# Optimization experiments

Measured on AMD Instinct MI355X. Metric: run time of the kernel, lower is better.

Reference implementation:

```python
import jax, jax.numpy as jnp
import numpy as np

NB_HEADS = 16
HEAD_DIM = 64
ATTN_LIM = 1024   # L: span of attention over past tokens
BLOCK = 512       # M: query block size
RAMP = 32         # attn_span_len: soft-mask ramp length
BATCH = 8         # sequences; merged leading dim is BATCH*NB_HEADS


def _skew(X, pad_value):
    # X: B x M x L  ->  B x M x (M+L), row i shifted right by i
    B, M, L = X.shape
    X = jnp.pad(X, ((0, 0), (0, 0), (0, M + 1)), constant_values=pad_value)
    X = X.reshape(B, M * (L + M + 1))[:, :-M]
    return X.reshape(B, M, M + L)


def _unskew(X):
    # X: B x M x (M+L)  ->  B x M x L, undo the diagonal shift
    B, M, ML = X.shape
    L = ML - M
    X = X.reshape(B, M * ML)
    X = jnp.pad(X, ((0, 0), (0, M)))
    X = X.reshape(B, M, ML + 1)
    return X[:, :, :L]


def setup_inputs() -> dict:
    key = jax.random.key(0)
    ks = jax.random.split(key, 5)
    B = BATCH * NB_HEADS
    M, L, H = BLOCK, ATTN_LIM, HEAD_DIM
    return {
        "query": jax.random.normal(ks[0], (B, M, H), jnp.float32),
        "key": jax.random.normal(ks[1], (B, M + L, H), jnp.float32),
        "value": jax.random.normal(ks[2], (B, M + L, H), jnp.float32),
        "key_pe": jax.random.normal(ks[3], (1, H, L), jnp.float32),
        "span_val": jax.random.uniform(ks[4], (NB_HEADS, 1, 1), jnp.float32),
    }


def reference(query, key, value, key_pe, span_val):
    B, M, H = query.shape
    L = key_pe.shape[-1]
    # content attention over the (M+L) cache window, unskewed to relative coords
    attn_cont = _unskew(jnp.matmul(query, jnp.swapaxes(key, -1, -2)))  # B x M x L
    attn_pos = jnp.matmul(query, key_pe)                               # B x M x L
    attn = (attn_cont + attn_pos) / jnp.sqrt(jnp.float32(H))
    attn = jax.nn.softmax(attn, axis=-1)
    # adaptive-span soft mask per head (AdaptiveMask), then renormalize
    z = jnp.clip(span_val, 0.0, 1.0)
    template = jnp.arange(1 - L, 1, dtype=jnp.float32)    # linspace(1-L, 0, L)
    mask = jnp.clip((template + z * jnp.float32(L)) / jnp.float32(RAMP) + 1.0,
                    0.0, 1.0)
    attn = attn.reshape(B // NB_HEADS, NB_HEADS, M, L) * mask[None]
    attn = attn / (attn.sum(-1, keepdims=True) + 1e-8)
    attn = attn.reshape(B, M, L)
    # skew back to absolute coords and contract with values
    out = jnp.matmul(_skew(attn, 0.0), value)             # B x M x H
    return out
```

## Files before the change

### kernel.cpp

```cpp
#include <hip/hip_runtime.h>
#include <hip/hip_bf16.h>

typedef __attribute__((ext_vector_type(8))) short short8;
typedef __attribute__((ext_vector_type(4))) float f32x4;

#define MFMA16(a, b, c) __builtin_amdgcn_mfma_f32_16x16x32_bf16((a), (b), (c), 0, 0, 0)
#define QSCALE 0.18033688f
#define EXP2F(x) __builtin_amdgcn_exp2f(x)

__device__ __forceinline__ unsigned short f2bf(float f) {
    unsigned u = __builtin_bit_cast(unsigned, f);
    u += 0x7FFFu + ((u >> 16) & 1u);
    return (unsigned short)(u >> 16);
}
__device__ __forceinline__ unsigned short bfc(float f) {
    return (unsigned short)((__builtin_bit_cast(unsigned, f) + 0x8000u) >> 16);
}

__device__ __forceinline__ short8 pack8(float4 a, float4 b) {
    short8 r;
    r[0] = (short)f2bf(a.x); r[1] = (short)f2bf(a.y);
    r[2] = (short)f2bf(a.z); r[3] = (short)f2bf(a.w);
    r[4] = (short)f2bf(b.x); r[5] = (short)f2bf(b.y);
    r[6] = (short)f2bf(b.z); r[7] = (short)f2bf(b.w);
    return r;
}
__device__ __forceinline__ short8 pack8s(float4 a, float4 b, float s) {
    short8 r;
    r[0] = (short)f2bf(a.x * s); r[1] = (short)f2bf(a.y * s);
    r[2] = (short)f2bf(a.z * s); r[3] = (short)f2bf(a.w * s);
    r[4] = (short)f2bf(b.x * s); r[5] = (short)f2bf(b.y * s);
    r[6] = (short)f2bf(b.z * s); r[7] = (short)f2bf(b.w * s);
    return r;
}

__device__ __forceinline__ void stage16(const void* g, void* l) {
    __builtin_amdgcn_global_load_lds((const __attribute__((address_space(1))) void*)g,
                                     (__attribute__((address_space(3))) void*)l, 16, 0, 0);
}
__device__ __forceinline__ float bpermf(int sa, float v) {
    return __builtin_bit_cast(float,
        __builtin_amdgcn_ds_bpermute(sa, __builtin_bit_cast(int, v)));
}

__global__ void conv_all_kernel(const float* __restrict__ K, const float* __restrict__ V,
                                const float* __restrict__ PE,
                                unsigned short* __restrict__ Kws,
                                unsigned short* __restrict__ Vws,
                                unsigned short* __restrict__ PET) {
    __shared__ unsigned short T[64][72];
    const int blk = blockIdx.x, tid = threadIdx.x;
    if (blk < 6144) {
        int idx = blk * 256 + tid;
        int jl = idx >> 3;
        int e0 = (idx & 7) << 3;
        int x  = (jl & 7) << 3;
        const float* src = K + ((size_t)jl << 6) + (e0 ^ x);
        float4 a = ((const float4*)src)[0], b = ((const float4*)src)[1];
        *(short8*)(Kws + ((size_t)jl << 6) + e0) = pack8(a, b);
    } else if (blk < 9216) {
        int blkv = blk - 6144;
        int b = blkv / 24, vb = blkv - b * 24;
        {
            int j = tid >> 2, h0 = (tid & 3) << 4;
            const float* src = V + ((size_t)(b * 1536 + vb * 64 + j) << 6) + h0;
            float4 a0 = ((const float4*)src)[0], a1 = ((const float4*)src)[1];
            float4 a2 = ((const float4*)src)[2], a3 = ((const float4*)src)[3];
            *(short8*)&T[j][h0]     = pack8(a0, a1);
            *(short8*)&T[j][h0 + 8] = pack8(a2, a3);
        }
        __syncthreads();
        {
            int h = tid & 63, k0 = (tid >> 6) << 4;
            int x = (h & 7) << 3;
            unsigned short* dst = Vws + ((size_t)(b * 24 + vb) << 12) + (h << 6) + k0;
            short8 o0, o1;
#pragma unroll
            for (int u = 0; u < 8; ++u) o0[u] = (short)T[(k0 + u) ^ x][h];
#pragma unroll
            for (int u = 0; u < 8; ++u) o1[u] = (short)T[(k0 + 8 + u) ^ x][h];
            ((short8*)dst)[0] = o0;
            ((short8*)dst)[1] = o1;
        }
    } else {
        int idx = (blk - 9216) * 256 + tid;
        int l = idx >> 6, h = idx & 63;
        PET[idx] = f2bf(PE[(h << 10) | l]);
    }
}

__global__ void pe_only_kernel(const float* __restrict__ pe,
                               unsigned short* __restrict__ pet) {
    int idx = blockIdx.x * 256 + threadIdx.x;
    int l = idx >> 6, h = idx & 63;
    pet[idx] = f2bf(pe[(h << 10) | l]);
}

__global__ __launch_bounds__(256, 4) void attn_v5(
    const float* __restrict__ Qg, const unsigned short* __restrict__ Kws,
    const unsigned short* __restrict__ Vws, const unsigned short* __restrict__ PET,
    const float* __restrict__ SPAN, float* __restrict__ OUT)
{
    __shared__ unsigned short Klds[2][4096];
    __shared__ unsigned short Vlds[2][4096];
    __shared__ unsigned short Wlds[4][1024];

    const int bid = blockIdx.x;
    const int b   = (bid & 7) * 16 + (bid >> 6);
    const int i0  = ((bid >> 3) & 7) << 6;
    const int tid = threadIdx.x, w = tid >> 6, lane = tid & 63;
    const int c16 = lane & 15, g = lane >> 4;

    float z = SPAN[b & 15];
    z = fminf(fmaxf(z, 0.f), 1.f);
    const float mc = z * 32.f + 1.f - 1023.f * 0.03125f;

    short8 qf0, qf1;
    {
        const float* qp = Qg + ((size_t)((b << 9) + i0 + (w << 4) + c16) << 6) + (g << 3);
        qf0 = pack8s(*(const float4*)qp,        *(const float4*)(qp + 4),  QSCALE);
        qf1 = pack8s(*(const float4*)(qp + 32), *(const float4*)(qp + 36), QSCALE);
    }

    const f32x4 zero = {0.f, 0.f, 0.f, 0.f};
    f32x4 Oacc[4] = {zero, zero, zero, zero};
    f32x4 sumw = zero, sume = zero;
    f32x4 Sp[5];

    const char* kbase = (const char*)Kws + (((size_t)b * 1536 + i0) << 7);
    const char* vbase = (const char*)Vws + (((size_t)b * 24 + (i0 >> 6)) << 13);
    const int ubase = w << 10;
    const int loff  = ubase + lane * 16;

    int bsrc[4];
#pragma unroll
    for (int r = 0; r < 4; ++r)
        bsrc[r] = ((lane & 48) | ((c16 - (g << 2) - r) & 15)) << 2;

#define STAGE(bufi, t) do {                                                    \
        const char* kg_ = kbase + (t) * 8192 + loff;                           \
        const char* vg_ = vbase + (t) * 8192 + loff;                           \
        unsigned short* kl_ = &Klds[bufi][ubase >> 1];                         \
        unsigned short* vl_ = &Vlds[bufi][ubase >> 1];                         \
        stage16(kg_, kl_); stage16(kg_ + 4096, kl_ + 2048);                    \
        stage16(vg_, vl_); stage16(vg_ + 4096, vl_ + 2048);                    \
    } while (0)

#define STRIP(dst, lbase) do {                                                 \
        int lr_ = (lbase) + c16;                                               \
        lr_ = lr_ < 0 ? 0 : (lr_ > 1023 ? 1023 : lr_);                         \
        const unsigned short* pp_ = PET + ((lr_ << 6) + (g << 3));             \
        short8 p0_ = *(const short8*)pp_;                                      \
        short8 p1_ = *(const short8*)(pp_ + 32);                               \
        f32x4 a_ = MFMA16(qf0, p0_, zero);                                     \
        dst = MFMA16(qf1, p1_, a_);                                            \
    } while (0)

    STAGE(0, 0);
    { const int lb0 = -(w << 4) - 16; STRIP(Sp[4], lb0); }

    for (int t = 0; t < 17; ++t) {
        const int buf = t & 1;
        __syncthreads();
        if (t < 16) STAGE(buf ^ 1, t + 1);

        const int d0w = (t << 6) - (w << 4);
        const int lb  = d0w - 16;
        const bool edge = (t == 0) || (t == 16);

        __builtin_amdgcn_s_setprio(1);
        f32x4 Sc[4];
        const int xk = (c16 & 7) << 3;
#pragma unroll
        for (int jc = 0; jc < 4; ++jc) {
            const unsigned short* p = &Klds[buf][(jc * 16 + c16) << 6];
            short8 k0 = *(const short8*)(p + ((g << 3) ^ xk));
            short8 k1 = *(const short8*)(p + (((g << 3) + 32) ^ xk));
            f32x4 a = MFMA16(qf0, k0, zero);
            Sc[jc] = MFMA16(qf1, k1, a);
        }
        Sp[0] = Sp[4];
        STRIP(Sp[1], lb + 16);
        STRIP(Sp[2], lb + 32);
        STRIP(Sp[3], lb + 48);
        STRIP(Sp[4], lb + 64);
        __builtin_amdgcn_s_setprio(0);

        unsigned short* Wp = &Wlds[w][0];
#pragma unroll
        for (int r = 0; r < 4; ++r) {
            const int ii    = (g << 2) + r;
            const int delta = c16 - ii;
            const int sa    = bsrc[r];
            float sh0 = bpermf(sa, Sp[0][r]);
            float sh1 = bpermf(sa, Sp[1][r]);
            float sh2 = bpermf(sa, Sp[2][r]);
            float sh3 = bpermf(sa, Sp[3][r]);
            float sh4 = bpermf(sa, Sp[4][r]);
            const bool lo_ = delta < 0;
            const int xw = (ii & 7) << 3;
            const int lbase = d0w + delta;
            const float mb = fmaf((float)lbase, 0.03125f, mc);
#pragma unroll
            for (int jc = 0; jc < 4; ++jc) {
                float pa, pb;
                if (jc == 0) { pa = sh0; pb = sh1; }
                else if (jc == 1) { pa = sh1; pb = sh2; }
                else if (jc == 2) { pa = sh2; pb = sh3; }
                else { pa = sh3; pb = sh4; }
                const float pe = lo_ ? pa : pb;
                float e = EXP2F(Sc[jc][r] + pe);
                if (edge) {
                    const int l_ = lbase + (jc << 4);
                    if ((unsigned)l_ >= 1024u) e = 0.f;
                }
                const float m_ = fminf(fmaxf(mb + 0.5f * jc, 0.f), 1.f);
                const float wgt = e * m_;
                sumw[r] += wgt;
                sume[r] += e;
                Wp[(ii << 6) + (((jc << 4) + c16) ^ xw)] = bfc(wgt);
            }
        }

        const int xr = (c16 & 7) << 3;
        const unsigned short* wrow = &Wlds[w][c16 << 6];
        short8 wf0 = *(const short8*)(wrow + ((g << 3) ^ xr));
        short8 wf1 = *(const short8*)(wrow + (((g << 3) + 32) ^ xr));
        __builtin_amdgcn_s_setprio(1);
#pragma unroll
        for (int ht = 0; ht < 4; ++ht) {
            const unsigned short* vr = &Vlds[buf][(ht * 16 + c16) << 6];
            short8 v0 = *(const short8*)(vr + ((g << 3) ^ xr));
            short8 v1 = *(const short8*)(vr + (((g << 3) + 32) ^ xr));
            f32x4 a = MFMA16(wf0, v0, Oacc[ht]);
            Oacc[ht] = MFMA16(wf1, v1, a);
        }
        __builtin_amdgcn_s_setprio(0);
    }

#pragma unroll
    for (int r = 0; r < 4; ++r) {
        float sw = sumw[r], se = sume[r];
#pragma unroll
        for (int m = 1; m < 16; m <<= 1) {
            sw += __shfl_xor(sw, m, 64);
            se += __shfl_xor(se, m, 64);
        }
        const float inv = 1.0f / (sw + 1e-8f * se);
        float* op = OUT + ((size_t)((b << 9) + i0 + (w << 4) + (g << 2) + r) << 6);
#pragma unroll
        for (int ht = 0; ht < 4; ++ht)
            op[ht * 16 + c16] = Oacc[ht][r] * inv;
    }
#undef STAGE
#undef STRIP
}

__global__ __launch_bounds__(256, 4) void attn_v1(
    const float* __restrict__ Qg, const float* __restrict__ Kg,
    const float* __restrict__ Vg, const unsigned short* __restrict__ PET,
    const float* __restrict__ SPAN, float* __restrict__ OUT)
{
    __shared__ unsigned short Klds[64 * 72];
    __shared__ unsigned short Vlds[64 * 72];
    __shared__ unsigned short Wlds[4][16 * 72];

    const int bid = blockIdx.x;
    const int b  = (bid & 7) * 16 + (bid >> 6);
    const int qt = (bid >> 3) & 7;
    const int i0 = qt << 6;
    const int tid = threadIdx.x, w = tid >> 6, lane = tid & 63;
    const int c16 = lane & 15, g = lane >> 4;

    float z = SPAN[b & 15];
    z = fminf(fmaxf(z, 0.0f), 1.0f);
    const float zc = z * 32.0f + 1.0f;

    short8 qf0, qf1;
    {
        const float* qp = Qg + ((size_t)(b * 512 + i0 + w * 16 + c16) * 64 + g * 8);
        qf0 = pack8(*(const float4*)qp,        *(const float4*)(qp + 4));
        qf1 = pack8(*(const float4*)(qp + 32), *(const float4*)(qp + 36));
    }
    const f32x4 zero = {0.f, 0.f, 0.f, 0.f};
    f32x4 Oacc[4] = {zero, zero, zero, zero};
    f32x4 sumw = zero, sume = zero;
    const int d0w_off = -(w << 4);

    for (int dblk = 0; dblk < 17; ++dblk) {
        const int d = dblk << 6;
        __syncthreads();
        {
            const int row = tid >> 2, h0 = (tid & 3) << 4;
            const float* kp = Kg + ((size_t)(b * 1536 + i0 + d + row) * 64 + h0);
            float4 k0 = ((const float4*)kp)[0], k1 = ((const float4*)kp)[1];
            float4 k2 = ((const float4*)kp)[2], k3 = ((const float4*)kp)[3];
            *(short8*)&Klds[row * 72 + h0]     = pack8(k0, k1);
            *(short8*)&Klds[row * 72 + h0 + 8] = pack8(k2, k3);
        }
        {
            const int j0 = (tid & 31) << 1, h0 = (tid >> 5) << 3;
            const float* vp = Vg + ((size_t)(b * 1536 + i0 + d + j0) * 64 + h0);
            float4 a0 = ((const float4*)vp)[0], a1 = ((const float4*)vp)[1];
            float4 b0 = ((const float4*)(vp + 64))[0], b1 = ((const float4*)(vp + 64))[1];
            float ta[8] = {a0.x, a0.y, a0.z, a0.w, a1.x, a1.y, a1.z, a1.w};
            float tb[8] = {b0.x, b0.y, b0.z, b0.w, b1.x, b1.y, b1.z, b1.w};
#pragma unroll
            for (int u = 0; u < 8; ++u) {
                unsigned pv = (unsigned)f2bf(ta[u]) | ((unsigned)f2bf(tb[u]) << 16);
                *(unsigned*)&Vlds[(h0 + u) * 72 + j0] = pv;
            }
        }
        __syncthreads();

        const int d0w = d + d0w_off;
        const int lb  = d0w - 16;
        f32x4 Sp[5];
#pragma unroll
        for (int tt = 0; tt < 5; ++tt) {
            int lr = lb + (tt << 4) + c16;
            lr = lr < 0 ? 0 : (lr > 1023 ? 1023 : lr);
            const unsigned short* pp = PET + ((lr << 6) + (g << 3));
            short8 p0 = *(const short8*)pp;
            short8 p1 = *(const short8*)(pp + 32);
            f32x4 acc = MFMA16(qf0, p0, zero);
            Sp[tt] = MFMA16(qf1, p1, acc);
        }
        f32x4 Sc[4];
#pragma unroll
        for (int jc = 0; jc < 4; ++jc) {
            const unsigned short* kb = &Klds[(jc * 16 + c16) * 72 + (g << 3)];
            short8 k0 = *(const short8*)kb;
            short8 k1 = *(const short8*)(kb + 32);
            f32x4 acc = MFMA16(qf0, k0, zero);
            Sc[jc] = MFMA16(qf1, k1, acc);
        }
        unsigned short* Wp = Wlds[w];
#pragma unroll
        for (int jc = 0; jc < 4; ++jc) {
#pragma unroll
            for (int r = 0; r < 4; ++r) {
                const int ii    = (g << 2) + r;
                const int delta = c16 - ii;
                const int src   = (lane & 48) | (delta & 15);
                const float pa  = __shfl(Sp[jc][r],     src, 64);
                const float pb  = __shfl(Sp[jc + 1][r], src, 64);
                const float pe  = (delta >= 0) ? pb : pa;
                const int l     = d0w + (jc << 4) + delta;
                const float sv  = (Sc[jc][r] + pe) * 0.125f;
                const float e   = __expf(sv);
                const bool valid = ((unsigned)l < 1024u);
                float msk = (float)(l - 1023) * 0.03125f + zc;
                msk = fminf(fmaxf(msk, 0.0f), 1.0f);
                const float wgt = valid ? e * msk : 0.0f;
                sumw[r] += wgt;
                sume[r] += valid ? e : 0.0f;
                Wp[ii * 72 + (jc << 4) + c16] = f2bf(wgt);
            }
        }
        short8 wf0 = *(const short8*)&Wp[c16 * 72 + (g << 3)];
        short8 wf1 = *(const short8*)&Wp[c16 * 72 + 32 + (g << 3)];
#pragma unroll
        for (int ht = 0; ht < 4; ++ht) {
            const unsigned short* vb = &Vlds[(ht * 16 + c16) * 72 + (g << 3)];
            short8 v0 = *(const short8*)vb;
            short8 v1 = *(const short8*)(vb + 32);
            f32x4 a = MFMA16(wf0, v0, Oacc[ht]);
            Oacc[ht] = MFMA16(wf1, v1, a);
        }
    }
#pragma unroll
    for (int r = 0; r < 4; ++r) {
        float sw = sumw[r], se = sume[r];
#pragma unroll
        for (int m = 1; m < 16; m <<= 1) {
            sw += __shfl_xor(sw, m, 64);
            se += __shfl_xor(se, m, 64);
        }
        const float inv = 1.0f / (sw + 1e-8f * se);
        float* op = OUT + ((size_t)(b * 512 + i0 + w * 16 + (g << 2) + r) * 64);
#pragma unroll
        for (int ht = 0; ht < 4; ++ht)
            op[ht * 16 + c16] = Oacc[ht][r] * inv;
    }
}

extern "C" void kernel_launch(void* const* d_in, const int* in_sizes, int n_in,
                              void* d_out, int out_size, void* d_ws, size_t ws_size,
                              hipStream_t stream) {
    const float* Q    = (const float*)d_in[0];
    const float* K    = (const float*)d_in[1];
    const float* V    = (const float*)d_in[2];
    const float* PE   = (const float*)d_in[3];
    const float* SPAN = (const float*)d_in[4];

    const size_t VWS_BYTES = (size_t)128 * 24 * 4096 * 2;
    const size_t KWS_BYTES = (size_t)128 * 1536 * 64 * 2;
    const size_t PET_BYTES = (size_t)1024 * 64 * 2;

    if (ws_size >= VWS_BYTES + KWS_BYTES + PET_BYTES) {
        unsigned short* Vws = (unsigned short*)d_ws;
        unsigned short* Kws = (unsigned short*)((char*)d_ws + VWS_BYTES);
        unsigned short* PET = (unsigned short*)((char*)d_ws + VWS_BYTES + KWS_BYTES);
        conv_all_kernel<<<9472, 256, 0, stream>>>(K, V, PE, Kws, Vws, PET);
        attn_v5<<<1024, 256, 0, stream>>>(Q, Kws, Vws, PET, SPAN, (float*)d_out);
    } else {
        unsigned short* PET = (unsigned short*)d_ws;
        pe_only_kernel<<<256, 256, 0, stream>>>(PE, PET);
        attn_v1<<<1024, 256, 0, stream>>>(Q, K, V, PET, SPAN, (float*)d_out);
    }
}
```

Baseline: 105.2 us.

## Reuse K LDS buffer for weights, prefetch PE fragments, target five waves

Removes the separate Wlds shared array by writing softmax weights into the current K buffer after an added barrier. This cuts LDS per block, and the waves_per_eu(5,5) attribute asks for higher occupancy. PE fragments for the next tile are loaded into registers one iteration ahead instead of being fetched just before their MFMAs, to hide global-load latency. The cost is an extra __syncthreads per iteration, more live registers for the prefetched fragments, and register pressure under the tighter occupancy target.

```diff
diff --git a/kernel.cpp b/kernel.cpp
--- a/kernel.cpp
+++ b/kernel.cpp
@@ -96,14 +96,15 @@
     pet[idx] = f2bf(pe[(h << 10) | l]);
 }
 
-__global__ __launch_bounds__(256, 4) void attn_v5(
+__global__ __launch_bounds__(256)
+__attribute__((amdgpu_waves_per_eu(5, 5)))
+void attn_v6(
     const float* __restrict__ Qg, const unsigned short* __restrict__ Kws,
     const unsigned short* __restrict__ Vws, const unsigned short* __restrict__ PET,
     const float* __restrict__ SPAN, float* __restrict__ OUT)
 {
     __shared__ unsigned short Klds[2][4096];
     __shared__ unsigned short Vlds[2][4096];
-    __shared__ unsigned short Wlds[4][1024];
 
     const int bid = blockIdx.x;
     const int b   = (bid & 7) * 16 + (bid >> 6);
@@ -126,6 +127,7 @@
     f32x4 Oacc[4] = {zero, zero, zero, zero};
     f32x4 sumw = zero, sume = zero;
     f32x4 Sp[5];
+    short8 ppf[4][2];
 
     const char* kbase = (const char*)Kws + (((size_t)b * 1536 + i0) << 7);
     const char* vbase = (const char*)Vws + (((size_t)b * 24 + (i0 >> 6)) << 13);
@@ -146,18 +148,29 @@
         stage16(vg_, vl_); stage16(vg_ + 4096, vl_ + 2048);                    \
     } while (0)
 
-#define STRIP(dst, lbase) do {                                                 \
-        int lr_ = (lbase) + c16;                                               \
-        lr_ = lr_ < 0 ? 0 : (lr_ > 1023 ? 1023 : lr_);                         \
-        const unsigned short* pp_ = PET + ((lr_ << 6) + (g << 3));             \
-        short8 p0_ = *(const short8*)pp_;                                      \
-        short8 p1_ = *(const short8*)(pp_ + 32);                               \
-        f32x4 a_ = MFMA16(qf0, p0_, zero);                                     \
-        dst = MFMA16(qf1, p1_, a_);                                            \
+#define PELOAD(tn) do {                                                        \
+        const int lbn_ = ((tn) << 6) - (w << 4);                               \
+        _Pragma("unroll")                                                      \
+        for (int s_ = 0; s_ < 4; ++s_) {                                       \
+            int lr_ = lbn_ + (s_ << 4) + c16;                                  \
+            lr_ = lr_ < 0 ? 0 : (lr_ > 1023 ? 1023 : lr_);                     \
+            const unsigned short* pp_ = PET + ((lr_ << 6) + (g << 3));         \
+            ppf[s_][0] = *(const short8*)pp_;                                  \
+            ppf[s_][1] = *(const short8*)(pp_ + 32);                           \
+        }                                                                      \
     } while (0)
 
     STAGE(0, 0);
-    { const int lb0 = -(w << 4) - 16; STRIP(Sp[4], lb0); }
+    PELOAD(0);
+    {
+        int lr = -(w << 4) - 16 + c16;
+        lr = lr < 0 ? 0 : lr;
+        const unsigned short* pp = PET + ((lr << 6) + (g << 3));
+        short8 p0 = *(const short8*)pp;
+        short8 p1 = *(const short8*)(pp + 32);
+        f32x4 a = MFMA16(qf0, p0, zero);
+        Sp[4] = MFMA16(qf1, p1, a);
+    }
 
     for (int t = 0; t < 17; ++t) {
         const int buf = t & 1;
@@ -165,7 +178,6 @@
         if (t < 16) STAGE(buf ^ 1, t + 1);
 
         const int d0w = (t << 6) - (w << 4);
-        const int lb  = d0w - 16;
         const bool edge = (t == 0) || (t == 16);
 
         __builtin_amdgcn_s_setprio(1);
@@ -180,13 +192,17 @@
             Sc[jc] = MFMA16(qf1, k1, a);
         }
         Sp[0] = Sp[4];
-        STRIP(Sp[1], lb + 16);
-        STRIP(Sp[2], lb + 32);
-        STRIP(Sp[3], lb + 48);
-        STRIP(Sp[4], lb + 64);
+#pragma unroll
+        for (int s = 0; s < 4; ++s) {
+            f32x4 a = MFMA16(qf0, ppf[s][0], zero);
+            Sp[s + 1] = MFMA16(qf1, ppf[s][1], a);
+        }
         __builtin_amdgcn_s_setprio(0);
 
-        unsigned short* Wp = &Wlds[w][0];
+        __syncthreads();
+        if (t < 16) PELOAD(t + 1);
+
+        unsigned short* Wp = &Klds[buf][w << 10];
 #pragma unroll
         for (int r = 0; r < 4; ++r) {
             const int ii    = (g << 2) + r;
@@ -223,7 +239,7 @@
         }
 
         const int xr = (c16 & 7) << 3;
-        const unsigned short* wrow = &Wlds[w][c16 << 6];
+        const unsigned short* wrow = Wp + (c16 << 6);
         short8 wf0 = *(const short8*)(wrow + ((g << 3) ^ xr));
         short8 wf1 = *(const short8*)(wrow + (((g << 3) + 32) ^ xr));
         __builtin_amdgcn_s_setprio(1);
@@ -253,7 +269,7 @@
             op[ht * 16 + c16] = Oacc[ht][r] * inv;
     }
 #undef STAGE
-#undef STRIP
+#undef PELOAD
 }
 
 __global__ __launch_bounds__(256, 4) void attn_v1(
@@ -403,7 +419,7 @@
         unsigned short* Kws = (unsigned short*)((char*)d_ws + VWS_BYTES);
         unsigned short* PET = (unsigned short*)((char*)d_ws + VWS_BYTES + KWS_BYTES);
         conv_all_kernel<<<9472, 256, 0, stream>>>(K, V, PE, Kws, Vws, PET);
-        attn_v5<<<1024, 256, 0, stream>>>(Q, Kws, Vws, PET, SPAN, (float*)d_out);
+        attn_v6<<<1024, 256, 0, stream>>>(Q, Kws, Vws, PET, SPAN, (float*)d_out);
     } else {
         unsigned short* PET = (unsigned short*)d_ws;
         pe_only_kernel<<<256, 256, 0, stream>>>(PE, PET);
```

New measurement: 257.8 us. 2.45x slower.
